# Performance work log

Measured on AMD Instinct MI355X. Metric: run time of the kernel, lower is better.

## Reference

```python
import jax, jax.numpy as jnp
import numpy as np

NOISE_SIGMA = 0.07
NOISE_TIMESTEPS = np.array([0, 1, 2, 3])
T, B, N_INP, N_REC, N_OUT = 256, 256, 128, 512, 64


def setup_inputs() -> dict:
    key = jax.random.key(0)
    ks = jax.random.split(key, 7)
    inputs = jax.random.normal(ks[0], (T, B, N_INP), dtype=jnp.float32)
    # Precomputed noise: randn*sigma at noise timesteps, zeros elsewhere
    noise = jnp.zeros((T, B, N_REC), dtype=jnp.float32)
    nz = jax.random.normal(ks[1], (len(NOISE_TIMESTEPS), B, N_REC), dtype=jnp.float32) * NOISE_SIGMA
    noise = noise.at[jnp.asarray(NOISE_TIMESTEPS)].set(nz)
    Wi = jax.random.normal(ks[2], (N_REC, N_INP), dtype=jnp.float32) / np.sqrt(N_INP)
    bi = jax.random.normal(ks[3], (N_REC,), dtype=jnp.float32) * 0.01
    # orthogonal recurrent init
    A = jax.random.normal(ks[4], (N_REC, N_REC), dtype=jnp.float32)
    Q, _ = jnp.linalg.qr(A)
    Wrec = Q.astype(jnp.float32)
    Wo = jax.random.normal(ks[5], (N_OUT, N_REC), dtype=jnp.float32) / np.sqrt(N_REC)
    bo = jax.random.normal(ks[6], (N_OUT,), dtype=jnp.float32) * 0.01
    return {"inputs": inputs, "noise": noise, "Wi": Wi, "bi": bi,
            "Wrec": Wrec, "Wo": Wo, "bo": bo}


def reference(inputs, noise, Wi, bi, Wrec, Wo, bo):
    # Precompute input projection for all timesteps: [T, B, n_rec]
    proj = jnp.einsum('tbi,ri->tbr', inputs, Wi) + bi

    def step(hidden, xs):
        p, nz = xs
        hidden = jax.nn.relu(p + hidden @ Wrec.T + nz)  # [B, n_rec]
        return hidden, hidden

    h0 = jnp.zeros((inputs.shape[1], Wrec.shape[0]), dtype=inputs.dtype)
    hidden, h = jax.lax.scan(step, h0, (proj, noise))
    output = jax.nn.softmax(hidden @ Wo.T + bo, axis=-1)  # [B, n_out]
    return output, h, hidden
```

## Files before the change

### kernel.cpp

```cpp
#include <hip/hip_runtime.h>
#include <hip/hip_bf16.h>
#include <stdint.h>

#define T_STEPS 256
#define B_SZ    256
#define NI      128
#define NR      512
#define NO      64
#define BT      16
#define HALF_R  256

typedef __attribute__((ext_vector_type(8))) short short8;
typedef __attribute__((ext_vector_type(4))) short short4v;
typedef __attribute__((ext_vector_type(4))) float f32x4;
typedef __attribute__((ext_vector_type(2))) unsigned long long u64x2;

__device__ __forceinline__ unsigned short f2bf(float f) {
    union { float f; unsigned u; } v; v.f = f;
    unsigned u = v.u;
    return (unsigned short)((u + 0x7FFFu + ((u >> 16) & 1u)) >> 16);
}

template<int KTB>
__device__ __forceinline__ void recur8(const unsigned char* Hbuf,
                                       const short8 (&Bh)[2][16],
                                       f32x4& acc0, f32x4& acc1,
                                       int l15, int l4, unsigned swzA) {
    #pragma unroll
    for (int kk = 0; kk < 8; ++kk) {
        const unsigned off = l15 * 1024 + (((unsigned)((KTB + kk) * 64 + l4 * 16)) ^ swzA);
        const short8 a = *(const short8*)(Hbuf + off);
        acc0 = __builtin_amdgcn_mfma_f32_16x16x32_bf16(a, Bh[0][KTB + kk], acc0, 0, 0, 0);
        acc1 = __builtin_amdgcn_mfma_f32_16x16x32_bf16(a, Bh[1][KTB + kk], acc1, 0, 0, 0);
    }
}

__global__ __launch_bounds__(256) void proj_gemm(
    const float* __restrict__ inputs, const float* __restrict__ Wi,
    const float* __restrict__ bi, const float* __restrict__ noise,
    float* __restrict__ proj)
{
    const int mb = blockIdx.x;
    const int nb = blockIdx.y;
    const int m0 = mb * 64, n0 = nb * 128;
    const int tid = threadIdx.x, w = tid >> 6, l = tid & 63;
    const int l15 = l & 15, l4 = l >> 4;

    __shared__ __align__(16) unsigned char Al[64 * 256];
    __shared__ __align__(16) unsigned char Wl[128 * 256];

    #pragma unroll
    for (int j = 0; j < 8; ++j) {
        const int f = j * 256 + tid;
        const int row = f >> 5, c4 = f & 31;
        const float4 v = *(const float4*)(inputs + (size_t)(m0 + row) * NI + c4 * 4);
        short4v pk;
        pk[0] = (short)f2bf(v.x); pk[1] = (short)f2bf(v.y);
        pk[2] = (short)f2bf(v.z); pk[3] = (short)f2bf(v.w);
        *(short4v*)(&Al[row * 256 + (((unsigned)(c4 * 8)) ^ ((row & 7) << 4))]) = pk;
    }
    #pragma unroll
    for (int j = 0; j < 16; ++j) {
        const int f = j * 256 + tid;
        const int r = f >> 5, c4 = f & 31;
        const float4 v = *(const float4*)(Wi + (size_t)(n0 + r) * NI + c4 * 4);
        short4v pk;
        pk[0] = (short)f2bf(v.x); pk[1] = (short)f2bf(v.y);
        pk[2] = (short)f2bf(v.z); pk[3] = (short)f2bf(v.w);
        *(short4v*)(&Wl[r * 256 + (((unsigned)(c4 * 8)) ^ ((r & 7) << 4))]) = pk;
    }
    __syncthreads();

    f32x4 acc[8];
    #pragma unroll
    for (int nt = 0; nt < 8; ++nt) acc[nt] = (f32x4){0.f, 0.f, 0.f, 0.f};
    #pragma unroll
    for (int kt = 0; kt < 4; ++kt) {
        const short8 a = *(const short8*)(
            &Al[(w * 16 + l15) * 256 + (((unsigned)(kt * 64 + l4 * 16)) ^ ((l15 & 7) << 4))]);
        #pragma unroll
        for (int nt = 0; nt < 8; ++nt) {
            const short8 b = *(const short8*)(
                &Wl[(nt * 16 + l15) * 256 + (((unsigned)(kt * 64 + l4 * 16)) ^ ((l15 & 7) << 4))]);
            acc[nt] = __builtin_amdgcn_mfma_f32_16x16x32_bf16(a, b, acc[nt], 0, 0, 0);
        }
    }

    const int t = m0 >> 8;
    #pragma unroll
    for (int nt = 0; nt < 8; ++nt) {
        const int n = n0 + nt * 16 + l15;
        const float bv = bi[n];
        #pragma unroll
        for (int q = 0; q < 4; ++q) {
            const int gr = m0 + w * 16 + l4 * 4 + q;
            float v = acc[nt][q] + bv;
            if (t < 4) v += noise[(size_t)gr * NR + n];
            proj[(size_t)gr * NR + n] = v;
        }
    }
}

__global__ __launch_bounds__(512) void rnn_scan(
    const float* __restrict__ Wrec,
    float* __restrict__ dout,
    unsigned* __restrict__ Xbuf,
    int* __restrict__ flags)
{
    const int bid  = blockIdx.x;
    const int grp  = bid & 15;
    const int half = bid >> 4;
    const int b0   = grp * BT;
    const int tid  = threadIdx.x;
    const int w    = tid >> 6;
    const int l    = tid & 63;
    const int l15  = l & 15;
    const int l4   = l >> 4;

    __shared__ __align__(16) unsigned char Hl[2][BT * 1024];

    short8 Bh[2][16];
    #pragma unroll
    for (int ct = 0; ct < 2; ++ct) {
        const int n = half * HALF_R + w * 32 + ct * 16 + l15;
        #pragma unroll
        for (int kt = 0; kt < 16; ++kt) {
            const float* src = Wrec + (size_t)n * NR + kt * 32 + l4 * 8;
            short8 f;
            #pragma unroll
            for (int j = 0; j < 8; ++j) f[j] = (short)f2bf(src[j]);
            Bh[ct][kt] = f;
        }
    }

    unsigned* Xg = Xbuf + (size_t)grp * 8192;
    int* myflag = flags + (grp * 2 + half) * 64;
    int* pflag  = flags + (grp * 2 + (half ^ 1)) * 64;

    float* hbuf   = dout + (size_t)NO * B_SZ;
    float* hidout = hbuf + (size_t)T_STEPS * B_SZ * NR;

    const unsigned swzA = (unsigned)((l15 & 7) << 4);
    const int n0 = half * HALF_R + w * 32 + l15;
    const int n1 = n0 + 16;
    const int mrow = l4 * 4;

    f32x4 acc0, acc1;
    #pragma unroll
    for (int q = 0; q < 4; ++q) {
        acc0[q] = hbuf[(size_t)(b0 + mrow + q) * NR + n0];
        acc1[q] = hbuf[(size_t)(b0 + mrow + q) * NR + n1];
    }

    float pj0[4], pj1[4];

    for (int t = 0; t < T_STEPS; ++t) {
        const int pn = (t & 1) ^ 1;

        if (t > 0) {
            if (half == 0) recur8<8>(&Hl[t & 1][0], Bh, acc0, acc1, l15, l4, swzA);
            else           recur8<0>(&Hl[t & 1][0], Bh, acc0, acc1, l15, l4, swzA);
        }

        float v0[4], v1[4];
        #pragma unroll
        for (int q = 0; q < 4; ++q) {
            v0[q] = fmaxf(acc0[q], 0.f);
            v1[q] = fmaxf(acc1[q], 0.f);
        }

        if (t == T_STEPS - 1) {
            #pragma unroll
            for (int q = 0; q < 4; ++q) {
                hbuf[((size_t)t * B_SZ + b0 + mrow + q) * NR + n0] = v0[q];
                hbuf[((size_t)t * B_SZ + b0 + mrow + q) * NR + n1] = v1[q];
                hidout[(size_t)(b0 + mrow + q) * NR + n0] = v0[q];
                hidout[(size_t)(b0 + mrow + q) * NR + n1] = v1[q];
            }
            break;
        }

        unsigned* Xreg = Xg + (pn * 2 + half) * 2048;
        #pragma unroll
        for (int ct = 0; ct < 2; ++ct) {
            #pragma unroll
            for (int q = 0; q < 4; ++q) {
                const float v = ct ? v1[q] : v0[q];
                const float other = __shfl_xor(v, 1, 64);
                if (!(l & 1)) {
                    const int m = mrow + q;
                    const int nloc = w * 32 + ct * 16 + l15;
                    const int nglob = half * HALF_R + nloc;
                    const unsigned pk = (unsigned)f2bf(v) | ((unsigned)f2bf(other) << 16);
                    const unsigned off = m * 1024 +
                        (((unsigned)(2 * nglob)) ^ ((unsigned)((m & 7) << 4)));
                    *(unsigned*)(&Hl[pn][off]) = pk;
                    const int j = nloc >> 1;
                    __hip_atomic_store(Xreg + (j >> 2) * 64 + m * 4 + (j & 3), pk,
                                       __ATOMIC_RELAXED, __HIP_MEMORY_SCOPE_AGENT);
                }
            }
        }
        asm volatile("s_waitcnt vmcnt(0)" ::: "memory");
        if (l == 0)
            __hip_atomic_fetch_add(myflag, 1, __ATOMIC_RELAXED, __HIP_MEMORY_SCOPE_AGENT);

        asm volatile("s_waitcnt lgkmcnt(0)" ::: "memory");
        __builtin_amdgcn_sched_barrier(0);
        __builtin_amdgcn_s_barrier();
        __builtin_amdgcn_sched_barrier(0);

        #pragma unroll
        for (int q = 0; q < 4; ++q) {
            pj0[q] = hbuf[((size_t)(t + 1) * B_SZ + b0 + mrow + q) * NR + n0];
            pj1[q] = hbuf[((size_t)(t + 1) * B_SZ + b0 + mrow + q) * NR + n1];
        }
        #pragma unroll
        for (int q = 0; q < 4; ++q) {
            hbuf[((size_t)t * B_SZ + b0 + mrow + q) * NR + n0] = v0[q];
            hbuf[((size_t)t * B_SZ + b0 + mrow + q) * NR + n1] = v1[q];
        }
        acc0 = (f32x4){0.f, 0.f, 0.f, 0.f};
        acc1 = (f32x4){0.f, 0.f, 0.f, 0.f};
        if (half == 0) recur8<0>(&Hl[pn][0], Bh, acc0, acc1, l15, l4, swzA);
        else           recur8<8>(&Hl[pn][0], Bh, acc0, acc1, l15, l4, swzA);

        const int target = 8 * (t + 1);
        int fv;
        while ((fv = __hip_atomic_load(pflag, __ATOMIC_RELAXED,
                                       __HIP_MEMORY_SCOPE_AGENT)) < target) {}
        asm volatile("" :: "v"(fv) : "memory");
        {
            const int c = tid >> 4, r = tid & 15;
            const unsigned* src = Xg + (pn * 2 + (half ^ 1)) * 2048 + c * 64 + r * 4;
            const unsigned long long d0 = __hip_atomic_load(
                (const unsigned long long*)src, __ATOMIC_RELAXED, __HIP_MEMORY_SCOPE_AGENT);
            const unsigned long long d1 = __hip_atomic_load(
                (const unsigned long long*)(src + 2), __ATOMIC_RELAXED, __HIP_MEMORY_SCOPE_AGENT);
            u64x2 dd; dd[0] = d0; dd[1] = d1;
            const unsigned off = r * 1024 +
                (((unsigned)((half ^ 1) * 512 + c * 16)) ^ ((unsigned)((r & 7) << 4)));
            *(u64x2*)(&Hl[pn][off]) = dd;
        }
        #pragma unroll
        for (int q = 0; q < 4; ++q) { acc0[q] += pj0[q]; acc1[q] += pj1[q]; }

        asm volatile("s_waitcnt lgkmcnt(0)" ::: "memory");
        __builtin_amdgcn_sched_barrier(0);
        __builtin_amdgcn_s_barrier();
        __builtin_amdgcn_sched_barrier(0);
    }
}

__global__ __launch_bounds__(256) void rnn_out(
    const float* __restrict__ Wo, const float* __restrict__ bo,
    float* __restrict__ dout)
{
    const float* hidden = dout + (size_t)NO * B_SZ + (size_t)T_STEPS * B_SZ * NR;
    const int b = blockIdx.x;
    const int tid = threadIdx.x, w = tid >> 6, l = tid & 63;

    __shared__ float hid[NR];
    __shared__ float lg[NO];

    if (tid < 128) {
        *(float4*)(&hid[tid * 4]) = *(const float4*)(hidden + (size_t)b * NR + tid * 4);
    }
    __syncthreads();

    #pragma unroll 1
    for (int jj = 0; jj < 16; ++jj) {
        const int j = w * 16 + jj;
        const float4* wr = (const float4*)(Wo + (size_t)j * NR + l * 8);
        const float4 a = wr[0], c = wr[1];
        const float4 h0 = *(const float4*)(&hid[l * 8]);
        const float4 h1 = *(const float4*)(&hid[l * 8 + 4]);
        float s = a.x * h0.x + a.y * h0.y + a.z * h0.z + a.w * h0.w
                + c.x * h1.x + c.y * h1.y + c.z * h1.z + c.w * h1.w;
        #pragma unroll
        for (int d = 32; d > 0; d >>= 1) s += __shfl_xor(s, d, 64);
        if (l == 0) lg[j] = s + bo[j];
    }
    __syncthreads();

    if (tid < 64) {
        const float x = lg[tid];
        float mx = x;
        #pragma unroll
        for (int d = 32; d > 0; d >>= 1) mx = fmaxf(mx, __shfl_xor(mx, d, 64));
        const float e = __expf(x - mx);
        float sum = e;
        #pragma unroll
        for (int d = 32; d > 0; d >>= 1) sum += __shfl_xor(sum, d, 64);
        dout[(size_t)b * NO + tid] = e / sum;
    }
}

extern "C" void kernel_launch(void* const* d_in, const int* in_sizes, int n_in,
                              void* d_out, int out_size, void* d_ws, size_t ws_size,
                              hipStream_t stream) {
    const float* inputs = (const float*)d_in[0];
    const float* noise  = (const float*)d_in[1];
    const float* Wi     = (const float*)d_in[2];
    const float* bi     = (const float*)d_in[3];
    const float* Wrec   = (const float*)d_in[4];
    const float* Wo     = (const float*)d_in[5];
    const float* bo     = (const float*)d_in[6];
    float* out = (float*)d_out;

    int* flags = (int*)d_ws;
    unsigned* Xbuf = (unsigned*)((char*)d_ws + 8192);

    float* proj = out + (size_t)NO * B_SZ;

    hipMemsetAsync(d_ws, 0, 8192, stream);
    proj_gemm<<<dim3(1024, 4), 256, 0, stream>>>(inputs, Wi, bi, noise, proj);
    rnn_scan<<<32, 512, 0, stream>>>(Wrec, out, Xbuf, flags);
    rnn_out<<<256, 256, 0, stream>>>(Wo, bo, out);
}
```

Before: 722.6 us.

## Replace flag-counter handshake with sign-bit tagged data polling between scan halves

The two blocks sharing a batch group used to exchange hidden-state halves through a store, a vmcnt drain, an atomic flag increment and a spin on the partner's flag before reading the data. Now the consumer polls the data words themselves. It relies on ReLU outputs having a zero bf16 sign bit and uses that bit as a per-use phase tag that alternates between double-buffer uses; the tag is masked off after arrival. Stores are also widened from 32-bit to 64-bit packed words using an extra shuffle. This removes one global round trip per timestep, at the cost of polling many words and depending on the outputs being non-negative.

```diff
diff --git a/kernel.cpp b/kernel.cpp
--- a/kernel.cpp
+++ b/kernel.cpp
@@ -104,8 +104,7 @@
 __global__ __launch_bounds__(512) void rnn_scan(
     const float* __restrict__ Wrec,
     float* __restrict__ dout,
-    unsigned* __restrict__ Xbuf,
-    int* __restrict__ flags)
+    unsigned long long* __restrict__ Xbuf)
 {
     const int bid  = blockIdx.x;
     const int grp  = bid & 15;
@@ -133,9 +132,7 @@
         }
     }
 
-    unsigned* Xg = Xbuf + (size_t)grp * 8192;
-    int* myflag = flags + (grp * 2 + half) * 64;
-    int* pflag  = flags + (grp * 2 + (half ^ 1)) * 64;
+    unsigned long long* Xg = Xbuf + (size_t)grp * 4096;
 
     float* hbuf   = dout + (size_t)NO * B_SZ;
     float* hidout = hbuf + (size_t)T_STEPS * B_SZ * NR;
@@ -156,6 +153,7 @@
 
     for (int t = 0; t < T_STEPS; ++t) {
         const int pn = (t & 1) ^ 1;
+        const int tag = ((t >> 1) & 1) ^ 1;
 
         if (t > 0) {
             if (half == 0) recur8<8>(&Hl[t & 1][0], Bh, acc0, acc1, l15, l4, swzA);
@@ -180,30 +178,32 @@
             break;
         }
 
-        unsigned* Xreg = Xg + (pn * 2 + half) * 2048;
-        #pragma unroll
-        for (int ct = 0; ct < 2; ++ct) {
+        {
+            unsigned long long* Xh = Xg + (size_t)(pn * 2 + half) * 1024;
+            const unsigned long long tagmask =
+                tag ? 0x8000800080008000ULL : 0ULL;
             #pragma unroll
-            for (int q = 0; q < 4; ++q) {
-                const float v = ct ? v1[q] : v0[q];
-                const float other = __shfl_xor(v, 1, 64);
-                if (!(l & 1)) {
-                    const int m = mrow + q;
-                    const int nloc = w * 32 + ct * 16 + l15;
-                    const int nglob = half * HALF_R + nloc;
-                    const unsigned pk = (unsigned)f2bf(v) | ((unsigned)f2bf(other) << 16);
-                    const unsigned off = m * 1024 +
-                        (((unsigned)(2 * nglob)) ^ ((unsigned)((m & 7) << 4)));
-                    *(unsigned*)(&Hl[pn][off]) = pk;
-                    const int j = nloc >> 1;
-                    __hip_atomic_store(Xreg + (j >> 2) * 64 + m * 4 + (j & 3), pk,
-                                       __ATOMIC_RELAXED, __HIP_MEMORY_SCOPE_AGENT);
+            for (int ct = 0; ct < 2; ++ct) {
+                #pragma unroll
+                for (int q = 0; q < 4; ++q) {
+                    const float v = ct ? v1[q] : v0[q];
+                    const float vo = __shfl_xor(v, 1, 64);
+                    unsigned pk = (unsigned)f2bf(v) | ((unsigned)f2bf(vo) << 16);
+                    const unsigned pk_hi = __shfl_xor(pk, 2, 64);
+                    if ((l & 3) == 0) {
+                        const int m = mrow + q;
+                        const int c = w * 32 + ct * 16 + l15;
+                        const unsigned long long val =
+                            (unsigned long long)pk | ((unsigned long long)pk_hi << 32);
+                        const unsigned off = m * 1024 +
+                            (((unsigned)(2 * (half * HALF_R + c))) ^ ((unsigned)((m & 7) << 4)));
+                        *(unsigned long long*)(&Hl[pn][off]) = val;
+                        __hip_atomic_store(Xh + m * 64 + (c >> 2), val | tagmask,
+                                           __ATOMIC_RELAXED, __HIP_MEMORY_SCOPE_AGENT);
+                    }
                 }
             }
         }
-        asm volatile("s_waitcnt vmcnt(0)" ::: "memory");
-        if (l == 0)
-            __hip_atomic_fetch_add(myflag, 1, __ATOMIC_RELAXED, __HIP_MEMORY_SCOPE_AGENT);
 
         asm volatile("s_waitcnt lgkmcnt(0)" ::: "memory");
         __builtin_amdgcn_sched_barrier(0);
@@ -225,21 +225,22 @@
         if (half == 0) recur8<0>(&Hl[pn][0], Bh, acc0, acc1, l15, l4, swzA);
         else           recur8<8>(&Hl[pn][0], Bh, acc0, acc1, l15, l4, swzA);
 
-        const int target = 8 * (t + 1);
-        int fv;
-        while ((fv = __hip_atomic_load(pflag, __ATOMIC_RELAXED,
-                                       __HIP_MEMORY_SCOPE_AGENT)) < target) {}
-        asm volatile("" :: "v"(fv) : "memory");
         {
-            const int c = tid >> 4, r = tid & 15;
-            const unsigned* src = Xg + (pn * 2 + (half ^ 1)) * 2048 + c * 64 + r * 4;
-            const unsigned long long d0 = __hip_atomic_load(
-                (const unsigned long long*)src, __ATOMIC_RELAXED, __HIP_MEMORY_SCOPE_AGENT);
-            const unsigned long long d1 = __hip_atomic_load(
-                (const unsigned long long*)(src + 2), __ATOMIC_RELAXED, __HIP_MEMORY_SCOPE_AGENT);
-            u64x2 dd; dd[0] = d0; dd[1] = d1;
-            const unsigned off = r * 1024 +
-                (((unsigned)((half ^ 1) * 512 + c * 16)) ^ ((unsigned)((r & 7) << 4)));
+            const int row = tid >> 5;
+            const unsigned kk = (unsigned)((2 * tid) & 63);
+            const unsigned long long* src =
+                Xg + (size_t)(pn * 2 + (half ^ 1)) * 1024 + row * 64 + kk;
+            const unsigned et = (unsigned)tag;
+            unsigned long long a, b;
+            for (;;) {
+                a = __hip_atomic_load(src,     __ATOMIC_RELAXED, __HIP_MEMORY_SCOPE_AGENT);
+                b = __hip_atomic_load(src + 1, __ATOMIC_RELAXED, __HIP_MEMORY_SCOPE_AGENT);
+                if ((((unsigned)(a >> 63)) == et) & (((unsigned)(b >> 63)) == et)) break;
+            }
+            if (tag) { a &= 0x7FFF7FFF7FFF7FFFULL; b &= 0x7FFF7FFF7FFF7FFFULL; }
+            u64x2 dd; dd[0] = a; dd[1] = b;
+            const unsigned off = row * 1024 +
+                (((unsigned)((half ^ 1) * 512 + kk * 8)) ^ ((unsigned)((row & 7) << 4)));
             *(u64x2*)(&Hl[pn][off]) = dd;
         }
         #pragma unroll
@@ -308,13 +309,12 @@
     const float* bo     = (const float*)d_in[6];
     float* out = (float*)d_out;
 
-    int* flags = (int*)d_ws;
-    unsigned* Xbuf = (unsigned*)((char*)d_ws + 8192);
+    unsigned long long* Xbuf = (unsigned long long*)d_ws;
 
     float* proj = out + (size_t)NO * B_SZ;
 
-    hipMemsetAsync(d_ws, 0, 8192, stream);
+    hipMemsetAsync(d_ws, 0, 16 * 4096 * sizeof(unsigned long long), stream);
     proj_gemm<<<dim3(1024, 4), 256, 0, stream>>>(inputs, Wi, bi, noise, proj);
-    rnn_scan<<<32, 512, 0, stream>>>(Wrec, out, Xbuf, flags);
+    rnn_scan<<<32, 512, 0, stream>>>(Wrec, out, Xbuf);
     rnn_out<<<256, 256, 0, stream>>>(Wo, bo, out);
 }
```

Result: faster. 683.6 us (-5.4%).
